# Performance work log

Measured on AMD Instinct MI355X. Metric: run time of the kernel, lower is better.

The kernel has to match this reference:

```python
import jax, jax.numpy as jnp
import numpy as np

D_MODEL = 1024
DIM_K = 128
DIM_V = 128

def setup_inputs() -> dict:
    key = jax.random.key(0)
    ks = jax.random.split(key, 8)
    B, T = 4, 2048
    s = 1.0 / np.sqrt(D_MODEL)
    return {
        "X_Q": jax.random.normal(ks[0], (B, T, D_MODEL), jnp.float32),
        "X_KV": jax.random.normal(ks[1], (B, T, D_MODEL), jnp.float32),
        "Wq": jax.random.normal(ks[2], (D_MODEL, DIM_K), jnp.float32) * s,
        "bq": jnp.zeros((DIM_K,), jnp.float32),
        "Wk": jax.random.normal(ks[3], (D_MODEL, DIM_K), jnp.float32) * s,
        "bk": jnp.zeros((DIM_K,), jnp.float32),
        "Wv": jax.random.normal(ks[4], (D_MODEL, DIM_V), jnp.float32) * s,
        "bv": jnp.zeros((DIM_V,), jnp.float32),
    }

def reference(X_Q, X_KV, Wq, bq, Wk, bk, Wv, bv):
    T = X_Q.shape[1]
    Q = X_Q @ Wq + bq                      # [B, T, dk]
    K = X_KV @ Wk + bk                     # [B, T, dk]
    V = X_KV @ Wv + bv                     # [B, T, dv]
    scale = 1.0 / jnp.sqrt(jnp.float32(DIM_K))
    scores = jnp.einsum('bqd,bkd->bqk', Q, K) * scale  # [B, T, T]
    causal = jnp.tril(jnp.ones((T, T), bool))
    scores = jnp.where(causal, scores, -jnp.inf)
    attn = jax.nn.softmax(scores, axis=-1)
    return jnp.einsum('bqk,bkd->bqd', attn, V)         # [B, T, dv]
```

## Files before the change

### kernel.cpp

```cpp
#include <hip/hip_runtime.h>
#include <hip/hip_bf16.h>
#include <math.h>

#define BT 8192
#define TT 2048
#define DM 1024
#define DK 128
#define NBLK 65

typedef __bf16 bf16x8 __attribute__((ext_vector_type(8)));
typedef float  f32x4  __attribute__((ext_vector_type(4)));
typedef unsigned short ushort4v __attribute__((ext_vector_type(4)));
typedef unsigned short ushort8v __attribute__((ext_vector_type(8)));

static __device__ __forceinline__ unsigned short f2bf(float x) {
    union { float f; unsigned u; } v; v.f = x;
    unsigned r = v.u + 0x7fffu + ((v.u >> 16) & 1u);
    return (unsigned short)(r >> 16);
}
static __device__ __forceinline__ float bf2f(unsigned short u) {
    union { unsigned u; float f; } v; v.u = (unsigned)u << 16;
    return v.f;
}

__host__ __device__ constexpr int slc_of(int q) { return (q == 0) ? 1 : ((q + 1) >> 1); }
__host__ __device__ constexpr int pfx_of(int q) { return (q == 0) ? 0 : 1 + (q * q - (q & 1)) / 4; }

#define QSCALE 0.1275312772629451f

__global__ __launch_bounds__(256) void wt_prep(
    const float* __restrict__ Wq, const float* __restrict__ Wk,
    const float* __restrict__ Wv, unsigned short* __restrict__ Wt)
{
    const int z = blockIdx.y;
    const float* __restrict__ W = (z == 0) ? Wq : (z == 1 ? Wk : Wv);
    const int k0 = blockIdx.x * 64;

    __shared__ __align__(16) __bf16 T[128][72];
    const int t = threadIdx.x;

#pragma unroll
    for (int jj = 0; jj < 8; ++jj) {
        int c  = jj * 256 + t;
        int k  = c >> 5;
        int n4 = (c & 31) * 4;
        float4 f = *reinterpret_cast<const float4*>(&W[(size_t)(k0 + k) * DK + n4]);
        T[n4 + 0][k] = (__bf16)f.x;
        T[n4 + 1][k] = (__bf16)f.y;
        T[n4 + 2][k] = (__bf16)f.z;
        T[n4 + 3][k] = (__bf16)f.w;
    }
    __syncthreads();

    const int n  = t >> 1;
    const int cb = (t & 1) * 32;
#pragma unroll
    for (int jj = 0; jj < 4; ++jj) {
        *reinterpret_cast<ushort8v*>(&Wt[((size_t)z * DK + n) * DM + k0 + cb + jj * 8]) =
            *reinterpret_cast<const ushort8v*>(&T[n][cb + jj * 8]);
    }
}

__global__ __launch_bounds__(256) void proj_mfma(
    const float* __restrict__ XQ, const float* __restrict__ XKV,
    const unsigned short* __restrict__ Wt,
    const float* __restrict__ bq, const float* __restrict__ bk,
    const float* __restrict__ bv,
    unsigned short* __restrict__ Qb, unsigned short* __restrict__ Kb,
    unsigned short* __restrict__ Vt)
{
    const int z = blockIdx.y;
    const float* __restrict__ X    = (z == 0) ? XQ : XKV;
    const float* __restrict__ bias = (z == 0) ? bq : (z == 1 ? bk : bv);
    const unsigned short* __restrict__ Wz = Wt + (size_t)z * DK * DM;

    __shared__ __align__(16) unsigned char lds_[2][24576];

    const int t    = threadIdx.x;
    const int lane = t & 63;
    const int wv   = t >> 6;
    const int i16  = lane & 15;
    const int g    = lane >> 4;
    const int wm   = wv >> 1;
    const int wn   = wv & 1;
    const int m0   = blockIdx.x * 32;

    f32x4 acc[4];
#pragma unroll
    for (int nt = 0; nt < 4; ++nt) acc[nt] = (f32x4){0.f, 0.f, 0.f, 0.f};

#define GLOADX(buf_, kk_)                                                      \
    {                                                                          \
        _Pragma("unroll")                                                      \
        for (int j = 0; j < 2; ++j) {                                          \
            const int s    = (wv * 2 + j) * 1024 + lane * 16;                  \
            const int row  = s >> 8;             \
            const int gran = (s >> 4) & 15;                                    \
            const float* gp = X + (size_t)(m0 + row) * DM + (kk_) * 64         \
                              + ((gran ^ (row & 15)) << 2);                    \
            __builtin_amdgcn_global_load_lds(                                  \
                (const unsigned int*)gp,                                       \
                (unsigned int*)&lds_[buf_][(wv * 2 + j) * 1024], 16, 0, 0);    \
        }                                                                      \
    }
#define GLOADW(buf_, kk_)                                                      \
    {                                                                          \
        _Pragma("unroll")                                                      \
        for (int j = 0; j < 4; ++j) {                                          \
            const int s    = (wv * 4 + j) * 1024 + lane * 16;                  \
            const int row  = s >> 7;             \
            const int gran = (s >> 4) & 7;                                     \
            const unsigned short* gp = Wz + (size_t)row * DM + (kk_) * 64      \
                              + ((gran ^ (row & 7)) << 3);                     \
            __builtin_amdgcn_global_load_lds(                                  \
                (const unsigned int*)gp,                                       \
                (unsigned int*)&lds_[buf_][8192 + (wv * 4 + j) * 1024],        \
                16, 0, 0);                                                     \
        }                                                                      \
    }
#define COMPUTE(buf_)                                                          \
    {                                                                          \
        const float*  Xl = (const float*)&lds_[buf_][0];                       \
        const __bf16* Wl = (const __bf16*)&lds_[buf_][8192];                   \
        _Pragma("unroll")                                                      \
        for (int c = 0; c < 2; ++c) {                                          \
            const int r   = wm * 16 + i16;                                     \
            const int gr0 = 8 * c + 2 * g;                                     \
            float4 x0 = *reinterpret_cast<const float4*>(                      \
                Xl + r * 64 + ((gr0 ^ (r & 15)) << 2));                        \
            float4 x1 = *reinterpret_cast<const float4*>(                      \
                Xl + r * 64 + (((gr0 + 1) ^ (r & 15)) << 2));                  \
            union { __bf16 b[8]; bf16x8 v; } u;                                \
            u.b[0] = (__bf16)x0.x; u.b[1] = (__bf16)x0.y;                      \
            u.b[2] = (__bf16)x0.z; u.b[3] = (__bf16)x0.w;                      \
            u.b[4] = (__bf16)x1.x; u.b[5] = (__bf16)x1.y;                      \
            u.b[6] = (__bf16)x1.z; u.b[7] = (__bf16)x1.w;                      \
            _Pragma("unroll")                                                  \
            for (int nt = 0; nt < 4; ++nt) {                                   \
                const int wr = wn * 64 + nt * 16 + i16;                        \
                bf16x8 wf = *reinterpret_cast<const bf16x8*>(                  \
                    Wl + wr * 64 + (((4 * c + g) ^ (wr & 7)) << 3));           \
                acc[nt] = __builtin_amdgcn_mfma_f32_16x16x32_bf16(             \
                    u.v, wf, acc[nt], 0, 0, 0);                                \
            }                                                                  \
        }                                                                      \
    }

    GLOADX(0, 0); GLOADW(0, 0);
    __syncthreads();

#pragma unroll
    for (int kk = 0; kk < 16; kk += 2) {
        GLOADX(1, kk + 1); GLOADW(1, kk + 1);
        COMPUTE(0);
        __syncthreads();
        if (kk + 2 < 16) { GLOADX(0, kk + 2); GLOADW(0, kk + 2); }
        COMPUTE(1);
        __syncthreads();
    }
#undef GLOADX
#undef GLOADW
#undef COMPUTE

    if (z == 0) {
#pragma unroll
        for (int nt = 0; nt < 4; ++nt) {
            int n = wn * 64 + nt * 16 + i16;
            float bb = bias[n];
#pragma unroll
            for (int r = 0; r < 4; ++r) {
                int mrow = m0 + wm * 16 + g * 4 + r;
                Qb[(size_t)mrow * DK + n] = f2bf((acc[nt][r] + bb) * QSCALE);
            }
        }
    } else if (z == 1) {
#pragma unroll
        for (int nt = 0; nt < 4; ++nt) {
            int n = wn * 64 + nt * 16 + i16;
            float bb = bias[n];
#pragma unroll
            for (int r = 0; r < 4; ++r) {
                int mrow = m0 + wm * 16 + g * 4 + r;
                Kb[(size_t)mrow * DK + n] = f2bf(acc[nt][r] + bb);
            }
        }
    } else {
        const int b  = m0 / TT;
        const int t0 = (m0 % TT) + wm * 16 + g * 4;
#pragma unroll
        for (int nt = 0; nt < 4; ++nt) {
            int d = wn * 64 + nt * 16 + i16;
            float bb = bias[d];
            ushort4v r;
#pragma unroll
            for (int e = 0; e < 4; ++e) r[e] = f2bf(acc[nt][e] + bb);
            *reinterpret_cast<ushort4v*>(&Vt[((size_t)b * DK + d) * TT + t0]) = r;
        }
    }
}

__global__ __launch_bounds__(512, 2) void attn_kernel(
    const unsigned short* __restrict__ Qb, const unsigned short* __restrict__ Kb,
    const unsigned short* __restrict__ Vt,
    unsigned short* __restrict__ pO, float* __restrict__ pMS)
{
    __shared__ __align__(16) unsigned short lds_[2][16384];

    const int t    = threadIdx.x;
    const int lane = t & 63;
    const int w    = t >> 6;
    const int qi   = lane & 15;
    const int g    = lane >> 4;

    const int bi    = blockIdx.x;
    const int batch = bi / NBLK;
    const int rr    = bi - batch * NBLK;
    int qbl = 0;
#pragma unroll
    for (int i = 1; i < 16; ++i) if (rr >= pfx_of(i)) qbl = i;
    const int slice = rr - (qbl == 0 ? 0 : 1 + (qbl * qbl - (qbl & 1)) / 4);
    const int S     = (qbl == 0) ? 1 : ((qbl + 1) >> 1);
    const int nch   = 2 * qbl + 2;
    const int q0    = qbl * 128;

    const unsigned short* __restrict__ Kbb = Kb + (size_t)batch * TT * DK;
    const unsigned short* __restrict__ Vtb = Vt + (size_t)batch * DK * TT;

    const int qrow  = q0 + w * 16 + qi;
    const int qminw = q0 + w * 16;
    const int qmaxw = q0 + w * 16 + 15;

    bf16x8 qf[4];
#pragma unroll
    for (int c = 0; c < 4; ++c)
        qf[c] = *reinterpret_cast<const bf16x8*>(
            &Qb[((size_t)batch * TT + qrow) * DK + c * 32 + g * 8]);

    f32x4 accO[8];
#pragma unroll
    for (int dt = 0; dt < 8; ++dt) accO[dt] = (f32x4){0.f, 0.f, 0.f, 0.f};
    float m = -1e30f, s = 0.f;

    ushort8v sreg[4];
    const int kslot0 = (w & 3) * 256;

#define STAGE_ISSUE(c_)                                                         \
    {                                                                           \
        const int k0s = (c_) * 64;                                              \
        if (w < 4) {                                                            \
            _Pragma("unroll")                                                   \
            for (int i = 0; i < 4; ++i) {                                       \
                int slot = kslot0 + i * 64 + lane;                              \
                int row  = slot >> 4;                                           \
                int colg = (slot & 15) ^ (row & 15);                            \
                sreg[i] = *reinterpret_cast<const ushort8v*>(                   \
                    &Kbb[(size_t)(k0s + row) * DK + colg * 8]);                 \
            }                                                                   \
        } else {                                                                \
            _Pragma("unroll")                                                   \
            for (int i = 0; i < 4; ++i) {                                       \
                int slot = kslot0 + i * 64 + lane;                              \
                int row  = slot >> 3;                                           \
                int colg = (slot & 7) ^ (row & 7);                              \
                sreg[i] = *reinterpret_cast<const ushort8v*>(                   \
                    &Vtb[(size_t)row * TT + k0s + colg * 8]);                   \
            }                                                                   \
        }                                                                       \
    }

#define STAGE_WRITE(buf_)                                                       \
    {                                                                           \
        const int base = (w < 4) ? 0 : 8192;                                    \
        _Pragma("unroll")                                                       \
        for (int i = 0; i < 4; ++i) {                                           \
            int slot = kslot0 + i * 64 + lane;                                  \
            *reinterpret_cast<ushort8v*>(&lds_[buf_][base + slot * 8]) = sreg[i]; \
        }                                                                       \
    }

    STAGE_ISSUE(slice);
    STAGE_WRITE(0);
    __syncthreads();

    int buf = 0;
    for (int c = slice; c < nch; c += S) {
        const int cn = c + S;
        if (cn < nch) STAGE_ISSUE(cn);

        const int k0 = c * 64;
        if (k0 <= qmaxw) {
            f32x4 accS[4];
#pragma unroll
            for (int ks = 0; ks < 4; ++ks) accS[ks] = (f32x4){0.f, 0.f, 0.f, 0.f};
#pragma unroll
            for (int cc = 0; cc < 4; ++cc) {
#pragma unroll
                for (int ks = 0; ks < 4; ++ks) {
                    bf16x8 kf = *reinterpret_cast<const bf16x8*>(
                        &lds_[buf][(ks * 16 + qi) * 128 + ((cc * 4 + g) ^ qi) * 8]);
                    accS[ks] = __builtin_amdgcn_mfma_f32_16x16x32_bf16(kf, qf[cc], accS[ks], 0, 0, 0);
                }
            }

            float xmax = -1e30f;
            if (k0 + 63 > qminw) {
#pragma unroll
                for (int ks = 0; ks < 4; ++ks)
#pragma unroll
                    for (int r = 0; r < 4; ++r) {
                        int k = k0 + ks * 16 + g * 4 + r;
                        float v0 = (k <= qrow) ? accS[ks][r] : -1e30f;
                        accS[ks][r] = v0;
                        xmax = fmaxf(xmax, v0);
                    }
            } else {
#pragma unroll
                for (int ks = 0; ks < 4; ++ks)
#pragma unroll
                    for (int r = 0; r < 4; ++r) xmax = fmaxf(xmax, accS[ks][r]);
            }

            if (__any(xmax > m + 8.f)) {
                xmax = fmaxf(xmax, __shfl_xor(xmax, 16));
                xmax = fmaxf(xmax, __shfl_xor(xmax, 32));
                float mn   = fmaxf(m, xmax);
                float corr = __builtin_amdgcn_exp2f(m - mn);
                s *= corr;
#pragma unroll
                for (int dt = 0; dt < 8; ++dt)
#pragma unroll
                    for (int e = 0; e < 4; ++e) accO[dt][e] *= corr;
                m = mn;
            }

            unsigned pk[8];
#pragma unroll
            for (int ks = 0; ks < 4; ++ks)
#pragma unroll
                for (int h = 0; h < 2; ++h) {
                    float plo = __builtin_amdgcn_exp2f(accS[ks][h * 2]     - m);
                    float phi = __builtin_amdgcn_exp2f(accS[ks][h * 2 + 1] - m);
                    s += plo + phi;
                    pk[ks * 2 + h] = (unsigned)f2bf(plo) | ((unsigned)f2bf(phi) << 16);
                }

            const int srcl0 = qi + 32 * (g & 1);
            bf16x8 pf[2];
#pragma unroll
            for (int c2 = 0; c2 < 2; ++c2) {
                union { unsigned u[4]; bf16x8 v; } pu;
#pragma unroll
                for (int w4 = 0; w4 < 4; ++w4) {
                    int srcl = srcl0 + 16 * (w4 >> 1);
                    int a = __shfl((int)pk[c2 * 4 + (w4 & 1)],     srcl);
                    int b = __shfl((int)pk[c2 * 4 + 2 + (w4 & 1)], srcl);
                    pu.u[w4] = (g & 2) ? (unsigned)b : (unsigned)a;
                }
                pf[c2] = pu.v;
            }

#pragma unroll
            for (int dt = 0; dt < 8; ++dt) {
#pragma unroll
                for (int c2 = 0; c2 < 2; ++c2) {
                    bf16x8 vf = *reinterpret_cast<const bf16x8*>(
                        &lds_[buf][8192 + (dt * 16 + qi) * 64 + ((c2 * 4 + g) ^ (qi & 7)) * 8]);
                    accO[dt] = __builtin_amdgcn_mfma_f32_16x16x32_bf16(vf, pf[c2], accO[dt], 0, 0, 0);
                }
            }
        }

        if (cn < nch) STAGE_WRITE(buf ^ 1);
        __syncthreads();
        buf ^= 1;
    }

    float srow = s + __shfl_xor(s, 16);
    srow += __shfl_xor(srow, 32);

    const size_t prow = (size_t)bi * 128 + w * 16 + qi;
    if (g == 0) {
        pMS[prow * 2]     = m;
        pMS[prow * 2 + 1] = srow;
    }
#pragma unroll
    for (int dt = 0; dt < 8; ++dt) {
        ushort4v r;
#pragma unroll
        for (int e = 0; e < 4; ++e) r[e] = f2bf(accO[dt][e]);
        *reinterpret_cast<ushort4v*>(&pO[prow * DK + dt * 16 + g * 4]) = r;
    }
#undef STAGE_ISSUE
#undef STAGE_WRITE
}

__global__ __launch_bounds__(256) void attn_combine(
    const unsigned short* __restrict__ pO, const float* __restrict__ pMS,
    float* __restrict__ O)
{
    const int t  = threadIdx.x;
    const int r  = blockIdx.x * 8 + (t >> 5);
    const int dq = (t & 31) * 4;

    const int batch = r >> 11;
    const int qbl   = (r >> 7) & 15;
    const int lr    = r & 127;
    const int S     = (qbl == 0) ? 1 : ((qbl + 1) >> 1);
    const int base  = batch * NBLK + (qbl == 0 ? 0 : 1 + (qbl * qbl - (qbl & 1)) / 4);

    float mstar = -1e30f;
    for (int ss = 0; ss < S; ++ss)
        mstar = fmaxf(mstar, pMS[((size_t)(base + ss) * 128 + lr) * 2]);

    float den = 0.f;
    float num[4] = {0.f, 0.f, 0.f, 0.f};
    for (int ss = 0; ss < S; ++ss) {
        const size_t pr = (size_t)(base + ss) * 128 + lr;
        float ms = pMS[pr * 2];
        float sv = pMS[pr * 2 + 1];
        float wgt = __builtin_amdgcn_exp2f(ms - mstar);
        den += wgt * sv;
        ushort4v ov = *reinterpret_cast<const ushort4v*>(&pO[pr * DK + dq]);
#pragma unroll
        for (int e = 0; e < 4; ++e) num[e] += wgt * bf2f(ov[e]);
    }

    const float inv = 1.f / den;
    float4 out;
    out.x = num[0] * inv; out.y = num[1] * inv;
    out.z = num[2] * inv; out.w = num[3] * inv;
    *reinterpret_cast<float4*>(&O[(size_t)r * DK + dq]) = out;
}

extern "C" void kernel_launch(void* const* d_in, const int* in_sizes, int n_in,
                              void* d_out, int out_size, void* d_ws, size_t ws_size,
                              hipStream_t stream) {
    const float* XQ  = (const float*)d_in[0];
    const float* XKV = (const float*)d_in[1];
    const float* Wq  = (const float*)d_in[2];
    const float* bq  = (const float*)d_in[3];
    const float* Wk  = (const float*)d_in[4];
    const float* bk  = (const float*)d_in[5];
    const float* Wv  = (const float*)d_in[6];
    const float* bv  = (const float*)d_in[7];

    unsigned short* Qb = (unsigned short*)d_ws;
    unsigned short* Kb = Qb + (size_t)BT * DK;
    unsigned short* Vt = Kb + (size_t)BT * DK;
    unsigned short* Wt = Vt + (size_t)BT * DK;
    float*          pMS = (float*)(Wt + (size_t)3 * DK * DM);
    unsigned short* pO  = (unsigned short*)(pMS + (size_t)4 * NBLK * 128 * 2);

    wt_prep<<<dim3(16, 3), 256, 0, stream>>>(Wq, Wk, Wv, Wt);

    proj_mfma<<<dim3(BT / 32, 3), 256, 0, stream>>>(
        XQ, XKV, Wt, bq, bk, bv, Qb, Kb, Vt);

    attn_kernel<<<dim3(4 * NBLK), 512, 0, stream>>>(Qb, Kb, Vt, pO, pMS);

    attn_combine<<<dim3(BT / 8), 256, 0, stream>>>(pO, pMS, (float*)d_out);
}
```

Before: 56.01 us.

## Give each wave private LDS staging and replace block barriers with vmcnt waits

The projection GEMM now gives each wave its own LDS region holding only the X rows and W columns it consumes. That makes double-buffering per-wave, so __syncthreads barriers can be replaced by s_waitcnt vmcnt on the wave's own async global-to-LDS loads. The K step shrinks to 32, and launch bounds ask for three blocks per CU. In exchange, X and W tiles shared between waves are now loaded redundantly, which raises global/L2 traffic. It also relies on the vmcnt counts matching the number of loads issued per stage.

```diff
diff --git a/kernel.cpp b/kernel.cpp
--- a/kernel.cpp
+++ b/kernel.cpp
@@ -61,7 +61,7 @@
     }
 }
 
-__global__ __launch_bounds__(256) void proj_mfma(
+__global__ __launch_bounds__(256, 3) void proj_mfma(
     const float* __restrict__ XQ, const float* __restrict__ XKV,
     const unsigned short* __restrict__ Wt,
     const float* __restrict__ bq, const float* __restrict__ bk,
@@ -74,7 +74,7 @@
     const float* __restrict__ bias = (z == 0) ? bq : (z == 1 ? bk : bv);
     const unsigned short* __restrict__ Wz = Wt + (size_t)z * DK * DM;
 
-    __shared__ __align__(16) unsigned char lds_[2][24576];
+    __shared__ __align__(16) unsigned char lds_[4][12288];
 
     const int t    = threadIdx.x;
     const int lane = t & 63;
@@ -89,78 +89,80 @@
 #pragma unroll
     for (int nt = 0; nt < 4; ++nt) acc[nt] = (f32x4){0.f, 0.f, 0.f, 0.f};
 
-#define GLOADX(buf_, kk_)                                                      \
+#define WAITV6 { asm volatile("s_waitcnt vmcnt(6)" ::: "memory"); \
+                 __builtin_amdgcn_sched_barrier(0); }
+#define WAITV0 { asm volatile("s_waitcnt vmcnt(0)" ::: "memory"); \
+                 __builtin_amdgcn_sched_barrier(0); }
+
+#define ISSUE(b_, kk_)                                                         \
     {                                                                          \
+                   \
         _Pragma("unroll")                                                      \
         for (int j = 0; j < 2; ++j) {                                          \
-            const int s    = (wv * 2 + j) * 1024 + lane * 16;                  \
-            const int row  = s >> 8;             \
-            const int gran = (s >> 4) & 15;                                    \
-            const float* gp = X + (size_t)(m0 + row) * DM + (kk_) * 64         \
-                              + ((gran ^ (row & 15)) << 2);                    \
+            const int s   = j * 1024 + lane * 16;                              \
+            const int lr  = s >> 7;                                            \
+            const int grn = (s >> 4) & 7;                                      \
+            const float* gp = X + (size_t)(m0 + wm * 16 + lr) * DM             \
+                              + (kk_) * 32 + ((grn ^ (lr & 7)) << 2);          \
             __builtin_amdgcn_global_load_lds(                                  \
                 (const unsigned int*)gp,                                       \
-                (unsigned int*)&lds_[buf_][(wv * 2 + j) * 1024], 16, 0, 0);    \
+                (unsigned int*)&lds_[wv][(b_) * 2048 + j * 1024], 16, 0, 0);   \
         }                                                                      \
-    }
-#define GLOADW(buf_, kk_)                                                      \
-    {                                                                          \
+                    \
         _Pragma("unroll")                                                      \
         for (int j = 0; j < 4; ++j) {                                          \
-            const int s    = (wv * 4 + j) * 1024 + lane * 16;                  \
-            const int row  = s >> 7;             \
-            const int gran = (s >> 4) & 7;                                     \
-            const unsigned short* gp = Wz + (size_t)row * DM + (kk_) * 64      \
-                              + ((gran ^ (row & 7)) << 3);                     \
+            const int s   = j * 1024 + lane * 16;                              \
+            const int lr  = s >> 6;                                            \
+            const int grn = (s >> 4) & 3;                                      \
+            const unsigned short* gp = Wz + (size_t)(wn * 64 + lr) * DM        \
+                              + (kk_) * 32 + ((grn ^ ((lr >> 1) & 3)) << 3);   \
             __builtin_amdgcn_global_load_lds(                                  \
                 (const unsigned int*)gp,                                       \
-                (unsigned int*)&lds_[buf_][8192 + (wv * 4 + j) * 1024],        \
+                (unsigned int*)&lds_[wv][4096 + (b_) * 4096 + j * 1024],       \
                 16, 0, 0);                                                     \
         }                                                                      \
     }
-#define COMPUTE(buf_)                                                          \
+
+#define COMPUTE(b_)                                                            \
     {                                                                          \
-        const float*  Xl = (const float*)&lds_[buf_][0];                       \
-        const __bf16* Wl = (const __bf16*)&lds_[buf_][8192];                   \
+        const unsigned char* Xb = &lds_[wv][(b_) * 2048];                      \
+        const unsigned char* Wb = &lds_[wv][4096 + (b_) * 4096];               \
+        f32x4 x0 = *reinterpret_cast<const f32x4*>(                            \
+            Xb + i16 * 128 + (((2 * g) ^ (i16 & 7)) << 4));                    \
+        f32x4 x1 = *reinterpret_cast<const f32x4*>(                            \
+            Xb + i16 * 128 + (((2 * g + 1) ^ (i16 & 7)) << 4));                \
+        union { __bf16 b[8]; bf16x8 v; } u;                                    \
+        u.b[0] = (__bf16)x0[0]; u.b[1] = (__bf16)x0[1];                        \
+        u.b[2] = (__bf16)x0[2]; u.b[3] = (__bf16)x0[3];                        \
+        u.b[4] = (__bf16)x1[0]; u.b[5] = (__bf16)x1[1];                        \
+        u.b[6] = (__bf16)x1[2]; u.b[7] = (__bf16)x1[3];                        \
         _Pragma("unroll")                                                      \
-        for (int c = 0; c < 2; ++c) {                                          \
-            const int r   = wm * 16 + i16;                                     \
-            const int gr0 = 8 * c + 2 * g;                                     \
-            float4 x0 = *reinterpret_cast<const float4*>(                      \
-                Xl + r * 64 + ((gr0 ^ (r & 15)) << 2));                        \
-            float4 x1 = *reinterpret_cast<const float4*>(                      \
-                Xl + r * 64 + (((gr0 + 1) ^ (r & 15)) << 2));                  \
-            union { __bf16 b[8]; bf16x8 v; } u;                                \
-            u.b[0] = (__bf16)x0.x; u.b[1] = (__bf16)x0.y;                      \
-            u.b[2] = (__bf16)x0.z; u.b[3] = (__bf16)x0.w;                      \
-            u.b[4] = (__bf16)x1.x; u.b[5] = (__bf16)x1.y;                      \
-            u.b[6] = (__bf16)x1.z; u.b[7] = (__bf16)x1.w;                      \
-            _Pragma("unroll")                                                  \
-            for (int nt = 0; nt < 4; ++nt) {                                   \
-                const int wr = wn * 64 + nt * 16 + i16;                        \
-                bf16x8 wf = *reinterpret_cast<const bf16x8*>(                  \
-                    Wl + wr * 64 + (((4 * c + g) ^ (wr & 7)) << 3));           \
-                acc[nt] = __builtin_amdgcn_mfma_f32_16x16x32_bf16(             \
-                    u.v, wf, acc[nt], 0, 0, 0);                                \
-            }                                                                  \
+        for (int nt = 0; nt < 4; ++nt) {                                       \
+            const int lr = nt * 16 + i16;                                      \
+            bf16x8 wf = *reinterpret_cast<const bf16x8*>(                      \
+                Wb + lr * 64 + ((g ^ ((lr >> 1) & 3)) << 4));                  \
+            acc[nt] = __builtin_amdgcn_mfma_f32_16x16x32_bf16(                 \
+                u.v, wf, acc[nt], 0, 0, 0);                                    \
         }                                                                      \
     }
 
-    GLOADX(0, 0); GLOADW(0, 0);
-    __syncthreads();
-
-#pragma unroll
-    for (int kk = 0; kk < 16; kk += 2) {
-        GLOADX(1, kk + 1); GLOADW(1, kk + 1);
+    ISSUE(0, 0);
+    ISSUE(1, 1);
+
+#pragma unroll
+    for (int kk = 0; kk < 32; kk += 2) {
+        WAITV6;
         COMPUTE(0);
-        __syncthreads();
-        if (kk + 2 < 16) { GLOADX(0, kk + 2); GLOADW(0, kk + 2); }
+        if (kk + 2 < 32) ISSUE(0, kk + 2);
+        if (kk + 3 < 32) { WAITV6; }
+        else             { WAITV0; }
         COMPUTE(1);
-        __syncthreads();
-    }
-#undef GLOADX
-#undef GLOADW
+        if (kk + 3 < 32) ISSUE(1, kk + 3);
+    }
+#undef ISSUE
 #undef COMPUTE
+#undef WAITV6
+#undef WAITV0
 
     if (z == 0) {
 #pragma unroll
```

New measurement: 68.22 us. 21.8% more time.

## Keep two k-tiles of async LDS loads in flight with explicit vmcnt waits

Applied to the files above, without the earlier changes.

Reworks the projection GEMM's double-buffered pipeline so both buffers are prefetched up front. Uses manual s_waitcnt vmcnt(6) waits and raw s_barrier calls in place of __syncthreads, so the next tile's global-to-LDS loads stay outstanding while the current tile is computed. Also adds a minimum-occupancy hint of 3 blocks per CU in the launch bounds. The risk is ordering bugs from the hand-placed waits and barriers, and register pressure from the occupancy hint.

```diff
diff --git a/kernel.cpp b/kernel.cpp
--- a/kernel.cpp
+++ b/kernel.cpp
@@ -61,7 +61,7 @@
     }
 }
 
-__global__ __launch_bounds__(256) void proj_mfma(
+__global__ __launch_bounds__(256, 3) void proj_mfma(
     const float* __restrict__ XQ, const float* __restrict__ XKV,
     const unsigned short* __restrict__ Wt,
     const float* __restrict__ bq, const float* __restrict__ bk,
@@ -89,7 +89,13 @@
 #pragma unroll
     for (int nt = 0; nt < 4; ++nt) acc[nt] = (f32x4){0.f, 0.f, 0.f, 0.f};
 
-#define GLOADX(buf_, kk_)                                                      \
+#define BARRIER { __builtin_amdgcn_s_barrier(); __builtin_amdgcn_sched_barrier(0); }
+#define WAIT6   { asm volatile("s_waitcnt vmcnt(6)" ::: "memory"); \
+                  __builtin_amdgcn_sched_barrier(0); }
+#define WAIT0   { asm volatile("s_waitcnt vmcnt(0)" ::: "memory"); \
+                  __builtin_amdgcn_sched_barrier(0); }
+
+#define ISSUE(b_, kk_)                                                         \
     {                                                                          \
         _Pragma("unroll")                                                      \
         for (int j = 0; j < 2; ++j) {                                          \
@@ -100,11 +106,8 @@
                               + ((gran ^ (row & 15)) << 2);                    \
             __builtin_amdgcn_global_load_lds(                                  \
                 (const unsigned int*)gp,                                       \
-                (unsigned int*)&lds_[buf_][(wv * 2 + j) * 1024], 16, 0, 0);    \
+                (unsigned int*)&lds_[b_][(wv * 2 + j) * 1024], 16, 0, 0);      \
         }                                                                      \
-    }
-#define GLOADW(buf_, kk_)                                                      \
-    {                                                                          \
         _Pragma("unroll")                                                      \
         for (int j = 0; j < 4; ++j) {                                          \
             const int s    = (wv * 4 + j) * 1024 + lane * 16;                  \
@@ -114,14 +117,15 @@
                               + ((gran ^ (row & 7)) << 3);                     \
             __builtin_amdgcn_global_load_lds(                                  \
                 (const unsigned int*)gp,                                       \
-                (unsigned int*)&lds_[buf_][8192 + (wv * 4 + j) * 1024],        \
+                (unsigned int*)&lds_[b_][8192 + (wv * 4 + j) * 1024],          \
                 16, 0, 0);                                                     \
         }                                                                      \
     }
-#define COMPUTE(buf_)                                                          \
+
+#define COMPUTE(b_)                                                            \
     {                                                                          \
-        const float*  Xl = (const float*)&lds_[buf_][0];                       \
-        const __bf16* Wl = (const __bf16*)&lds_[buf_][8192];                   \
+        const float*  Xl = (const float*)&lds_[b_][0];                         \
+        const __bf16* Wl = (const __bf16*)&lds_[b_][8192];                     \
         _Pragma("unroll")                                                      \
         for (int c = 0; c < 2; ++c) {                                          \
             const int r   = wm * 16 + i16;                                     \
@@ -146,21 +150,29 @@
         }                                                                      \
     }
 
-    GLOADX(0, 0); GLOADW(0, 0);
-    __syncthreads();
+    ISSUE(0, 0);
+    ISSUE(1, 1);
 
 #pragma unroll
     for (int kk = 0; kk < 16; kk += 2) {
-        GLOADX(1, kk + 1); GLOADW(1, kk + 1);
+        WAIT6;
+        BARRIER;
         COMPUTE(0);
-        __syncthreads();
-        if (kk + 2 < 16) { GLOADX(0, kk + 2); GLOADW(0, kk + 2); }
+        BARRIER;
+        if (kk + 2 < 16) ISSUE(0, kk + 2);
+        if (kk + 2 < 16) { WAIT6; } else { WAIT0; }
+        BARRIER;
         COMPUTE(1);
-        __syncthreads();
-    }
-#undef GLOADX
-#undef GLOADW
+        if (kk + 3 < 16) {
+            BARRIER;
+            ISSUE(1, kk + 3);
+        }
+    }
+#undef ISSUE
 #undef COMPUTE
+#undef BARRIER
+#undef WAIT6
+#undef WAIT0
 
     if (z == 0) {
 #pragma unroll
```

Result: slower. 58.54 us (+4.5%).
